# Kernel optimization log

Hardware: AMD Instinct MI355X
Metric: run time of the kernel (lower is better)

The kernel has to match this reference:

```python
import jax, jax.numpy as jnp
import numpy as np

BIG, SMALL = 13, 3
NK = 5                       # ceil(BIG / SMALL)
PADDING = SMALL - 1          # 2
EXTRA_PAD = PADDING - SMALL // 2   # 1
G = 2                        # group_in
C_OUT = 96
C_IN = G * C_OUT * NK        # 960
B, H, W = 16, 56, 56


def setup_inputs() -> dict:
    key = jax.random.key(0)
    k1, k2 = jax.random.split(key, 2)
    rng = np.random.default_rng(0)
    mid = BIG // 2
    real_pad = np.array([mid - i * SMALL - PADDING for i in range(NK)], dtype=np.int32)  # [4,1,-2,-5,-8]

    def perm_pads():
        # per output channel, a random permutation of the nk shift offsets
        return np.concatenate([rng.permutation(real_pad) for _ in range(C_OUT)])

    ph = np.stack([perm_pads() for _ in range(G)])  # (G, C_OUT*NK) horizontal shifts
    pv = np.stack([perm_pads() for _ in range(G)])  # (G, C_OUT*NK) vertical shifts
    pad_hv = np.concatenate([ph, pv], axis=0).T.astype(np.int32)  # (C_OUT*NK, 2*G)

    ids = []
    for _ in range(G):
        col = []
        for _ in range(C_OUT):
            arr = -np.ones(NK, dtype=np.int32)
            pos = rng.choice(NK, min(4, NK), replace=False)
            arr[pos] = np.arange(min(4, NK))
            col.append(arr)
        ids.append(np.concatenate(col))
    idx_identit = np.stack(ids).T.astype(np.int32)  # (C_OUT*NK, G)

    x = jax.random.normal(k1, (B, C_IN, H, W), jnp.float32)
    proj_w = jax.random.normal(k2, (C_OUT, C_IN), jnp.float32) * np.float32(1.0 / np.sqrt(C_IN))
    return {
        'x': x,
        'pad_hv': jnp.asarray(pad_hv),
        'idx_identit': jnp.asarray(idx_identit),
        'local_scale': jnp.ones((1, C_IN, 1, 1), jnp.float32),
        'local_bias': jnp.zeros((1, C_IN, 1, 1), jnp.float32),
        'proj_w': proj_w,
        'fuse_alpha': jnp.float32(0.7),
        'b': B, 'hout': H, 'wout': W,
    }


def reference(x, pad_hv, idx_identit, local_scale, local_bias, proj_w, fuse_alpha, b, hout, wout):
    p = EXTRA_PAD
    xp = jnp.pad(x, ((0, 0), (0, 0), (p, p), (p, p)), mode='edge')  # replicate pad
    Bx, Cin, Hp, Wp = xp.shape

    # per-channel shift offsets: channel ic = g*C_OUT*NK + slot, slot = co*NK + k
    ph = pad_hv[:, :G].T.reshape(-1)  # (C_IN,) horizontal (w-axis) shifts
    pv = pad_hv[:, G:].T.reshape(-1)  # (C_IN,) vertical (h-axis) shifts

    def gather_w(xc, s):  # xc: (B, Hp, Wp), s: scalar int shift
        idx = jnp.arange(wout) + p + s
        valid = ((idx >= 0) & (idx < Wp)).astype(xc.dtype)
        return xc[:, p:p + hout, jnp.clip(idx, 0, Wp - 1)] * valid[None, None, :]

    def gather_h(xc, s):
        idx = jnp.arange(hout) + p + s
        valid = ((idx >= 0) & (idx < Hp)).astype(xc.dtype)
        return xc[:, jnp.clip(idx, 0, Hp - 1), p:p + wout] * valid[None, :, None]

    xh = jax.vmap(gather_w, in_axes=(1, 0), out_axes=1)(xp, ph)  # (B, C_IN, hout, wout)
    xv = jax.vmap(gather_h, in_axes=(1, 0), out_axes=1)(xp, pv)
    x1 = xh.reshape(Bx, G, C_OUT, NK, hout, wout).sum((1, 3))    # horizontal-shift group
    x2 = xv.reshape(Bx, G, C_OUT, NK, hout, wout).sum((1, 3))    # vertical-shift group

    id_mask = (idx_identit.T.reshape(-1) >= 0).astype(xp.dtype)  # (C_IN,) identity slots
    x3 = (xp[:, :, p:p + hout, p:p + wout] * id_mask[None, :, None, None])
    x3 = x3.reshape(Bx, G, C_OUT, NK, hout, wout).sum((1, 3))    # identity group

    global_feat = (x1 + x2 + x3) / 3.0

    local = xp * (local_scale + 1e-5) + local_bias
    local = jax.image.resize(local, (Bx, Cin, hout, wout), method='bilinear')  # align_corners=False
    local = jnp.einsum('bchw,oc->bohw', local, proj_w)  # 1x1 conv, no bias

    return fuse_alpha * global_feat + (1.0 - fuse_alpha) * local
```

## Files before the change

kernel.cpp:

```cpp
#include <hip/hip_runtime.h>
#include <hip/hip_bf16.h>
#include <cstdint>
#include <cstddef>

#define B_    16
#define CIN   960
#define HH    56
#define WW_   56
#define GG    2
#define COUT  96
#define NK_   5
#define PIX   3136
#define NCH   30

#define WF_OFF   0
#define BIAS_OFF 61440
#define Y_OFF    61568

typedef __attribute__((ext_vector_type(8))) short bf16x8;
typedef __attribute__((ext_vector_type(4))) float f32x4;

__device__ __forceinline__ short f2b(float f) {
    union { float f; unsigned u; } c; c.f = f;
    unsigned r = (c.u + 0x7FFFu + ((c.u >> 16) & 1u)) >> 16;
    return (short)r;
}
__device__ __forceinline__ float b2f(short s) {
    union { unsigned u; float f; } c;
    c.u = ((unsigned)(unsigned short)s) << 16;
    return c.f;
}

#define GLOAD_LDS16(gp, lp)                                                        \
    __builtin_amdgcn_global_load_lds(                                              \
        (const __attribute__((address_space(1))) unsigned*)(gp),                   \
        (__attribute__((address_space(3))) unsigned*)(lp), 16, 0, 0)

__global__ void prep_wb(const float* __restrict__ pw, const float* __restrict__ sc,
                        short* __restrict__ wf) {
    int idx = blockIdx.x * 256 + threadIdx.x;
    if (idx >= NCH * 6 * 64) return;
    const int lane = idx & 63;
    const int nf   = idx >> 6;
    const int f    = nf % 6;
    const int n    = nf / 6;
    const int o    = f * 16 + (lane & 15);
    const int c0   = n * 32 + (lane >> 4) * 8;
    bf16x8 v;
#pragma unroll
    for (int k = 0; k < 8; ++k)
        v[k] = f2b(pw[o * CIN + c0 + k] * (sc[c0 + k] + 1e-5f));
    *(bf16x8*)((char*)wf + (size_t)n * 8192 + (f * 64 + lane) * 16) = v;
}

__global__ void prep_bias(const float* __restrict__ pw, const float* __restrict__ bi,
                          float* __restrict__ bias) {
    const int o = blockIdx.x;
    const int l = threadIdx.x;
    float s = 0.f;
    for (int c = l; c < CIN; c += 64) s += pw[o * CIN + c] * bi[c];
#pragma unroll
    for (int off = 32; off; off >>= 1) s += __shfl_down(s, off);
    if (l == 0) bias[o] = s;
}

__global__ __launch_bounds__(512)
void conv_mfma(const float* __restrict__ x, const short* __restrict__ wf,
               short* __restrict__ yb) {
    const int tid  = threadIdx.x;
    const int lane = tid & 63;
    const int wv   = tid >> 6;
    const int m    = wv >> 2;
    const int n    = wv & 3;
    const int b    = blockIdx.y;
    const int px0  = blockIdx.x * 64;

    __shared__ __align__(16) char xsb[3 * 8192];
    __shared__ __align__(16) char wlb[3 * 8192];

    const float* xbase = x + (size_t)b * CIN * PIX + px0;
    const char*  wfB   = (const char*)wf;

    const int sch  = wv * 4 + (lane >> 4);
    const int sS   = (wv >> 1) & 3;
    const int soff = (((lane >> 2) & 3) ^ sS) * 16 + (lane & 3) * 4;
    const int wsub = wv * 1024 + lane * 16;

    const int kb    = lane >> 4;
    const int bcol  = (lane & 15) * 4;
    const int bslot = ((n ^ kb) & 3) * 64;
    const int babs  = kb * 2048 + bslot + bcol;
    const int abase = m * 3072 + lane * 16;

    f32x4 acc0 = {0.f, 0.f, 0.f, 0.f};
    f32x4 acc1 = {0.f, 0.f, 0.f, 0.f};
    f32x4 acc2 = {0.f, 0.f, 0.f, 0.f};

#define STAGE(BS, c0)                                                            \
    {                                                                            \
        GLOAD_LDS16(xbase + (size_t)((c0) + sch) * PIX + soff,                   \
                    xsb + (BS) * 8192 + wv * 1024);                              \
        GLOAD_LDS16(wfB + (size_t)((c0) >> 5) * 8192 + wsub,                     \
                    wlb + (BS) * 8192 + wv * 1024);                              \
    }

    STAGE(0, 0);
    STAGE(1, 32);

#define STEP(n_, BI, BS, VM)                                                     \
    {                                                                            \
        asm volatile("s_waitcnt vmcnt(" #VM ")" ::: "memory");                   \
        asm volatile("s_barrier" ::: "memory");                                  \
        bf16x8 bfrag;                                                            \
        _Pragma("unroll")                                                        \
        for (int k = 0; k < 8; ++k)                                              \
            bfrag[k] = f2b(*(const float*)(xsb + (BI) * 8192 + babs + k * 256)); \
        const bf16x8 af0 = *(const bf16x8*)(wlb + (BI) * 8192 + abase);          \
        const bf16x8 af1 = *(const bf16x8*)(wlb + (BI) * 8192 + abase + 1024);   \
        const bf16x8 af2 = *(const bf16x8*)(wlb + (BI) * 8192 + abase + 2048);   \
        if ((n_) + 2 < NCH) STAGE(BS, ((n_) + 2) * 32);                          \
        acc0 = __builtin_amdgcn_mfma_f32_16x16x32_bf16(af0, bfrag, acc0, 0,0,0); \
        acc1 = __builtin_amdgcn_mfma_f32_16x16x32_bf16(af1, bfrag, acc1, 0,0,0); \
        acc2 = __builtin_amdgcn_mfma_f32_16x16x32_bf16(af2, bfrag, acc2, 0,0,0); \
    }

#pragma unroll 1
    for (int mm = 0; mm < 9; ++mm) {
        const int n0 = mm * 3;
        STEP(n0 + 0, 0, 2, 2);
        STEP(n0 + 1, 1, 0, 2);
        STEP(n0 + 2, 2, 1, 2);
    }
    STEP(27, 0, 2, 2);
    STEP(28, 1, 0, 2);
    STEP(29, 2, 1, 0);
#undef STEP
#undef STAGE

    short* yp = yb + (size_t)b * COUT * PIX + px0 + n * 16 + (lane & 15);
    const int o0 = m * 48 + (lane >> 4) * 4;
#pragma unroll
    for (int r = 0; r < 4; ++r) yp[(size_t)(o0 +      r) * PIX] = f2b(acc0[r]);
#pragma unroll
    for (int r = 0; r < 4; ++r) yp[(size_t)(o0 + 16 + r) * PIX] = f2b(acc1[r]);
#pragma unroll
    for (int r = 0; r < 4; ++r) yp[(size_t)(o0 + 32 + r) * PIX] = f2b(acc2[r]);
}

__device__ __forceinline__ void rweights56(int o, short* idx, float* wt) {
    const float ratio = 58.0f / 56.0f;
    const float kinv  = 56.0f / 58.0f;
    const float sf = ((float)o + 0.5f) * ratio - 0.5f;
    const int f0 = (int)floorf(sf);
    float sum = 0.f;
#pragma unroll
    for (int t = 0; t < 4; ++t) {
        int i = f0 - 1 + t;
        float w = fmaxf(1.0f - fabsf(sf - (float)i) * kinv, 0.0f);
        if (i < 0 || i > 57) w = 0.0f;
        idx[t] = (short)min(HH - 1, max(0, i - 1));
        wt[t] = w;
        sum += w;
    }
    const float inv = 1.0f / sum;
#pragma unroll
    for (int t = 0; t < 4; ++t) wt[t] *= inv;
}

__global__ __launch_bounds__(256)
void finalize(const float* __restrict__ x, const int* __restrict__ pad_hv,
              const int* __restrict__ idt, const short* __restrict__ yb,
              const float* __restrict__ bias, const float* __restrict__ alpha_p,
              float* __restrict__ out) {
    const int bc = blockIdx.x;
    const int co = bc % COUT;
    const int b  = bc / COUT;
    const int t  = threadIdx.x;

    __shared__ float  ylds[PIX];
    __shared__ float4 wt4[56];
    __shared__ short4 id4[56];
    __shared__ int   ish[10], isv[10], ipl[10];
    __shared__ float fid[10];

    if (t < 10) {
        const int g = t / 5;
        const int k = t - g * 5;
        const int slot = co * NK_ + k;
        ish[t] = pad_hv[slot * 4 + g];
        isv[t] = pad_hv[slot * 4 + 2 + g];
        fid[t] = (idt[slot * 2 + g] >= 0) ? 1.f : 0.f;
        ipl[t] = (g * (COUT * NK_) + slot) * PIX;
    }
    if (t < 56) {
        short ii[4]; float ww[4];
        rweights56(t, ii, ww);
        wt4[t] = make_float4(ww[0], ww[1], ww[2], ww[3]);
        id4[t] = make_short4(ii[0], ii[1], ii[2], ii[3]);
    }
    {
        const short* yp = yb + (size_t)bc * PIX;
#pragma unroll 1
        for (int i = t; i < PIX / 4; i += 256) {
            const short4 s4 = *(const short4*)(yp + i * 4);
            *(float4*)(ylds + i * 4) =
                make_float4(b2f(s4.x), b2f(s4.y), b2f(s4.z), b2f(s4.w));
        }
    }
    __syncthreads();

    int   ish_r[10], isv_r[10], ipl_r[10];
    float fid_r[10];
#pragma unroll
    for (int p = 0; p < 10; ++p) {
        ish_r[p] = ish[p]; isv_r[p] = isv[p];
        ipl_r[p] = ipl[p]; fid_r[p] = fid[p];
    }

    const float alpha = alpha_p[0];
    const float ia    = 1.0f - alpha;
    const float bco   = bias[co];
    const float* xb = x + (size_t)b * CIN * PIX;
    float* op = out + (size_t)bc * PIX;

#pragma unroll 1
    for (int px = t; px < PIX; px += 256) {
        const int h = (px * 18725) >> 20;
        const int w = px - h * WW_;
        const int hrow = px - w;

        float accg = 0.f;
#pragma unroll
        for (int p = 0; p < 10; ++p) {
            const float* xc = xb + ipl_r[p];
            const int jw = w + ish_r[p];
            const float mh = (jw >= -1 && jw <= WW_) ? 1.f : 0.f;
            accg += mh * xc[hrow + min(WW_ - 1, max(0, jw))];

            const int iv = h + isv_r[p];
            const float mv = (iv >= -1 && iv <= HH) ? 1.f : 0.f;
            accg += mv * xc[min(HH - 1, max(0, iv)) * WW_ + w];

            accg += fid_r[p] * xc[px];
        }

        const float4 ww4 = wt4[w];
        const short4 iw4 = id4[w];
        const float4 wh4 = wt4[h];
        const short4 ih4 = id4[h];
        float accl = 0.f;
#pragma unroll
        for (int a = 0; a < 4; ++a) {
            const int row = ((const short*)&ih4)[a] * WW_;
            const float* yr = ylds + row;
            float rs;
            rs = ww4.x * yr[iw4.x];
            rs = fmaf(ww4.y, yr[iw4.y], rs);
            rs = fmaf(ww4.z, yr[iw4.z], rs);
            rs = fmaf(ww4.w, yr[iw4.w], rs);
            accl = fmaf(((const float*)&wh4)[a], rs, accl);
        }
        accl += bco;

        op[px] = alpha * accg * (1.0f / 3.0f) + ia * accl;
    }
}

extern "C" void kernel_launch(void* const* d_in, const int* in_sizes, int n_in,
                              void* d_out, int out_size, void* d_ws, size_t ws_size,
                              hipStream_t stream) {
    const float* x      = (const float*)d_in[0];
    const int*   pad_hv = (const int*)d_in[1];
    const int*   idt    = (const int*)d_in[2];
    const float* lsc    = (const float*)d_in[3];
    const float* lbi    = (const float*)d_in[4];
    const float* pw     = (const float*)d_in[5];
    const float* alpha  = (const float*)d_in[6];
    float* out = (float*)d_out;

    float* ws   = (float*)d_ws;
    short* wf   = (short*)(ws + WF_OFF);
    float* bias = ws + BIAS_OFF;
    short* yb   = (short*)(ws + Y_OFF);

    prep_wb<<<(NCH * 6 * 64 + 255) / 256, 256, 0, stream>>>(pw, lsc, wf);
    prep_bias<<<COUT, 64, 0, stream>>>(pw, lbi, bias);
    conv_mfma<<<dim3(PIX / 64, B_), 512, 0, stream>>>(x, wf, yb);
    finalize<<<B_ * COUT, 256, 0, stream>>>(x, pad_hv, idt, yb, bias, alpha, out);
}
```

Before: 93.50 us.

## Emit bf16 copy of x from conv kernel and read it in finalize

The conv kernel now writes out the bf16-converted x values it already builds for its MFMA B fragments, as a full bf16 copy of x in workspace. Finalize then gathers from this half-width copy instead of the fp32 input, halving the bytes it reads for the shift and identity sums. In exchange the conv kernel issues many scattered 2-byte global stores, and the waitcnt counts and pipeline stage order are changed to account for them. The global-feature path also loses precision because it now sums bf16-rounded inputs.

After: 239.6 us. +156.2%, slower.

```diff
diff --git a/kernel.cpp b/kernel.cpp
--- a/kernel.cpp
+++ b/kernel.cpp
@@ -16,6 +16,7 @@
 #define WF_OFF   0
 #define BIAS_OFF 61440
 #define Y_OFF    61568
+#define XB_OFF   2470016
 
 typedef __attribute__((ext_vector_type(8))) short bf16x8;
 typedef __attribute__((ext_vector_type(4))) float f32x4;
@@ -66,7 +67,7 @@
 
 __global__ __launch_bounds__(512)
 void conv_mfma(const float* __restrict__ x, const short* __restrict__ wf,
-               short* __restrict__ yb) {
+               short* __restrict__ yb, short* __restrict__ xb) {
     const int tid  = threadIdx.x;
     const int lane = tid & 63;
     const int wv   = tid >> 6;
@@ -91,6 +92,9 @@
     const int bslot = ((n ^ kb) & 3) * 64;
     const int babs  = kb * 2048 + bslot + bcol;
     const int abase = m * 3072 + lane * 16;
+
+    short* const xstb = xb + (size_t)b * CIN * PIX + px0 + n * 16 + (lane & 15);
+    const int mk4 = m * 4;
 
     f32x4 acc0 = {0.f, 0.f, 0.f, 0.f};
     f32x4 acc1 = {0.f, 0.f, 0.f, 0.f};
@@ -119,21 +123,29 @@
         const bf16x8 af1 = *(const bf16x8*)(wlb + (BI) * 8192 + abase + 1024);   \
         const bf16x8 af2 = *(const bf16x8*)(wlb + (BI) * 8192 + abase + 2048);   \
         if ((n_) + 2 < NCH) STAGE(BS, ((n_) + 2) * 32);                          \
+        _Pragma("unroll")                                                        \
+        for (int j = 0; j < 4; ++j) {                                            \
+            const short dj = (m == 0) ? bfrag[j] : bfrag[4 + j];                 \
+            short* sp = xstb + (size_t)((n_) * 32 + kb * 8 + mk4 + j) * PIX;     \
+            asm volatile("global_store_short %0, %1, off"                        \
+                         :: "v"(sp), "v"((unsigned)(unsigned short)dj)           \
+                         : "memory");                                            \
+        }                                                                        \
         acc0 = __builtin_amdgcn_mfma_f32_16x16x32_bf16(af0, bfrag, acc0, 0,0,0); \
         acc1 = __builtin_amdgcn_mfma_f32_16x16x32_bf16(af1, bfrag, acc1, 0,0,0); \
         acc2 = __builtin_amdgcn_mfma_f32_16x16x32_bf16(af2, bfrag, acc2, 0,0,0); \
     }
 
+    STEP(0, 0, 2, 2);
+    STEP(1, 1, 0, 6);
 #pragma unroll 1
     for (int mm = 0; mm < 9; ++mm) {
-        const int n0 = mm * 3;
-        STEP(n0 + 0, 0, 2, 2);
-        STEP(n0 + 1, 1, 0, 2);
-        STEP(n0 + 2, 2, 1, 2);
-    }
-    STEP(27, 0, 2, 2);
-    STEP(28, 1, 0, 2);
-    STEP(29, 2, 1, 0);
+        const int n0 = 2 + mm * 3;
+        STEP(n0 + 0, 2, 1, 10);
+        STEP(n0 + 1, 0, 2, 10);
+        STEP(n0 + 2, 1, 0, 10);
+    }
+    STEP(29, 2, 1, 8);
 #undef STEP
 #undef STAGE
 
@@ -168,7 +180,7 @@
 }
 
 __global__ __launch_bounds__(256)
-void finalize(const float* __restrict__ x, const int* __restrict__ pad_hv,
+void finalize(const short* __restrict__ xb, const int* __restrict__ pad_hv,
               const int* __restrict__ idt, const short* __restrict__ yb,
               const float* __restrict__ bias, const float* __restrict__ alpha_p,
               float* __restrict__ out) {
@@ -220,7 +232,7 @@
     const float alpha = alpha_p[0];
     const float ia    = 1.0f - alpha;
     const float bco   = bias[co];
-    const float* xb = x + (size_t)b * CIN * PIX;
+    const short* xbb = xb + (size_t)b * CIN * PIX;
     float* op = out + (size_t)bc * PIX;
 
 #pragma unroll 1
@@ -232,16 +244,16 @@
         float accg = 0.f;
 #pragma unroll
         for (int p = 0; p < 10; ++p) {
-            const float* xc = xb + ipl_r[p];
+            const short* xc = xbb + ipl_r[p];
             const int jw = w + ish_r[p];
             const float mh = (jw >= -1 && jw <= WW_) ? 1.f : 0.f;
-            accg += mh * xc[hrow + min(WW_ - 1, max(0, jw))];
+            accg += mh * b2f(xc[hrow + min(WW_ - 1, max(0, jw))]);
 
             const int iv = h + isv_r[p];
             const float mv = (iv >= -1 && iv <= HH) ? 1.f : 0.f;
-            accg += mv * xc[min(HH - 1, max(0, iv)) * WW_ + w];
-
-            accg += fid_r[p] * xc[px];
+            accg += mv * b2f(xc[min(HH - 1, max(0, iv)) * WW_ + w]);
+
+            accg += fid_r[p] * b2f(xc[px]);
         }
 
         const float4 ww4 = wt4[w];
@@ -282,9 +294,10 @@
     short* wf   = (short*)(ws + WF_OFF);
     float* bias = ws + BIAS_OFF;
     short* yb   = (short*)(ws + Y_OFF);
+    short* xb16 = (short*)(ws + XB_OFF);
 
     prep_wb<<<(NCH * 6 * 64 + 255) / 256, 256, 0, stream>>>(pw, lsc, wf);
     prep_bias<<<COUT, 64, 0, stream>>>(pw, lbi, bias);
-    conv_mfma<<<dim3(PIX / 64, B_), 512, 0, stream>>>(x, wf, yb);
-    finalize<<<B_ * COUT, 256, 0, stream>>>(x, pad_hv, idt, yb, bias, alpha, out);
-}
+    conv_mfma<<<dim3(PIX / 64, B_), 512, 0, stream>>>(x, wf, yb, xb16);
+    finalize<<<B_ * COUT, 256, 0, stream>>>(xb16, pad_hv, idt, yb, bias, alpha, out);
+}
```
